# Optimization experiments

Measured on AMD Instinct MI355X. Metric: run time of the kernel, lower is better.

## Reference

```python
import jax, jax.numpy as jnp
import numpy as np

BETA = 0.25
EPS = 1e-10


def setup_inputs() -> dict:
    key = jax.random.key(0)
    k1, k2 = jax.random.split(key)
    z = jax.random.normal(k1, (16, 256, 32, 32), dtype=jnp.float32)
    # Original init: uniform(-1/n_embed, 1/n_embed)
    n_embed, embed_dim = 8192, 256
    codebook = jax.random.uniform(k2, (n_embed, embed_dim), dtype=jnp.float32,
                                  minval=-1.0 / n_embed, maxval=1.0 / n_embed)
    return {"z": z, "codebook": codebook}


def reference(z, codebook):
    B, C, H, W = z.shape
    n_embed = codebook.shape[0]
    zp = jnp.transpose(z, (0, 2, 3, 1))            # (B,H,W,C)
    zf = zp.reshape(-1, C)                          # (N,C)
    # squared L2 distances (N, n_embed)
    d = (jnp.sum(zf * zf, axis=1, keepdims=True)
         + jnp.sum(codebook * codebook, axis=1)
         - 2.0 * zf @ codebook.T)
    idx = jnp.argmin(d, axis=1)                     # (N,)
    zq = codebook[idx].reshape(zp.shape)            # gather == one-hot @ codebook
    commitment_loss = jnp.mean((jax.lax.stop_gradient(zq) - zp) ** 2)
    embedding_loss = jnp.mean((zq - jax.lax.stop_gradient(zp)) ** 2)
    loss = embedding_loss + BETA * commitment_loss
    # straight-through estimator
    zq_st = zp + jax.lax.stop_gradient(zq - zp)
    # perplexity from mean one-hot usage (counts / N)
    counts = jnp.zeros((n_embed,), dtype=zf.dtype).at[idx].add(1.0)
    avg_probs = counts / zf.shape[0]
    perplexity = jnp.exp(-jnp.sum(avg_probs * jnp.log(avg_probs + EPS)))
    zq_out = jnp.transpose(zq_st, (0, 3, 1, 2))     # (B,C,H,W)
    return zq_out, loss, perplexity, idx
```

## Files before the change

kernel.cpp:

```cpp
#include <hip/hip_runtime.h>
#include <math.h>

#define Nrows 16384
#define NE 8192
#define Kdim 256
#define HWsz 1024
#define NSPL 4
#define BETAF 0.25f
#define NLOSSBLK 4096

typedef __attribute__((ext_vector_type(8))) short bf16x8;
typedef __attribute__((ext_vector_type(16))) float f32x16;
typedef unsigned short u16;

__device__ inline u16 bf16_rne(float x) {
  unsigned int u = __float_as_uint(x);
  return (u16)((u + 0x7FFFu + ((u >> 16) & 1u)) >> 16);
}
__device__ inline float bf16_tof(u16 h) {
  return __uint_as_float(((unsigned int)h) << 16);
}
__device__ inline void gll16(const void* g, void* l) {
  __builtin_amdgcn_global_load_lds(
      (const __attribute__((address_space(1))) unsigned int*)g,
      (__attribute__((address_space(3))) unsigned int*)l, 16, 0, 0);
}

__global__ __launch_bounds__(256) void cc_kernel(const float* __restrict__ cb,
                                                 float* __restrict__ cc) {
  int wave = threadIdx.x >> 6;
  int lane = threadIdx.x & 63;
  int row = blockIdx.x * 4 + wave;
  const float4 v = *(const float4*)(cb + (size_t)row * Kdim + lane * 4);
  float s = v.x * v.x + v.y * v.y + v.z * v.z + v.w * v.w;
  for (int off = 32; off; off >>= 1) s += __shfl_down(s, off);
  if (lane == 0) cc[row] = s;
}

__global__ __launch_bounds__(256) void conv_cb(const float* __restrict__ cb,
                                               u16* __restrict__ Cf) {
  const int g = blockIdx.x * 256 + threadIdx.x;
  const int j = g >> 4, k16 = g & 15;
  const float* src = cb + (size_t)j * Kdim + k16 * 16;
  float f[16];
#pragma unroll
  for (int q = 0; q < 4; ++q) {
    const float4 v = ((const float4*)src)[q];
    f[q * 4 + 0] = v.x; f[q * 4 + 1] = v.y; f[q * 4 + 2] = v.z; f[q * 4 + 3] = v.w;
  }
  u16 h[3][16];
#pragma unroll
  for (int i = 0; i < 16; ++i) {
    const u16 q0 = bf16_rne(f[i]);
    const float r1 = f[i] - bf16_tof(q0);
    const u16 q1 = bf16_rne(r1);
    const float r2 = r1 - bf16_tof(q1);
    h[0][i] = q0; h[1][i] = q1; h[2][i] = bf16_rne(r2);
  }
  const int j32 = j >> 5, li = j & 31;
#pragma unroll
  for (int arr = 0; arr < 3; ++arr) {
#pragma unroll
    for (int kh = 0; kh < 2; ++kh) {
      const size_t off = ((size_t)(j32 * 3 + arr) * 16 + k16) * 512 + (kh * 32 + li) * 8;
      *(int4*)(Cf + off) = *(int4*)&h[arr][kh * 8];
    }
  }
}

__global__ __launch_bounds__(256) void conv_z(const float* __restrict__ z,
                                              u16* __restrict__ Zf,
                                              float* __restrict__ zz) {
  __shared__ float tile[64][68];
  const int t = threadIdx.x;
  const int bid = blockIdx.x;
  const int n0 = bid * 64;
  const int b = bid >> 4;
  const int hw0 = (bid & 15) << 6;
  const float* zb = z + (size_t)b * (Kdim * HWsz) + hw0;
  float zzacc = 0.f;
  const int rr = t >> 2;
  const int kq = (t & 3) * 16;
  for (int kc = 0; kc < 4; ++kc) {
#pragma unroll
    for (int i = 0; i < 16; ++i) {
      const int idx = i * 256 + t;
      const int k = idx >> 6, r = idx & 63;
      tile[r][k] = zb[(size_t)(kc * 64 + k) * HWsz + r];
    }
    __syncthreads();
    if (t < 64) {
      for (int k = 0; k < 64; ++k) {
        const float a = tile[t][k];
        zzacc = fmaf(a, a, zzacc);
      }
    }
    u16 h[3][16];
#pragma unroll
    for (int i = 0; i < 16; ++i) {
      const float fv = tile[rr][kq + i];
      const u16 q0 = bf16_rne(fv);
      const float r1 = fv - bf16_tof(q0);
      const u16 q1 = bf16_rne(r1);
      const float r2 = r1 - bf16_tof(q1);
      h[0][i] = q0; h[1][i] = q1; h[2][i] = bf16_rne(r2);
    }
    const int k16 = kc * 4 + (t & 3);
    const int n32 = bid * 2 + (rr >> 5), li = rr & 31;
#pragma unroll
    for (int arr = 0; arr < 3; ++arr) {
#pragma unroll
      for (int kh = 0; kh < 2; ++kh) {
        const size_t off = ((size_t)(n32 * 3 + arr) * 16 + k16) * 512 + (kh * 32 + li) * 8;
        *(int4*)(Zf + off) = *(int4*)&h[arr][kh * 8];
      }
    }
    __syncthreads();
  }
  if (t < 64) zz[n0 + t] = zzacc;
}

__global__ __launch_bounds__(256, 2) void vq_gemm(
    const u16* __restrict__ Cf, const u16* __restrict__ Zf,
    const float* __restrict__ cc, const float* __restrict__ zz,
    float* __restrict__ pd, int* __restrict__ pj) {
  __shared__ __align__(16) u16 Al[3][12288];
  __shared__ float ccs[2048];

  const int t = threadIdx.x;
  const int lane = t & 63;
  const int w = __builtin_amdgcn_readfirstlane(t >> 6);
  const int bid = blockIdx.x;
  const int cg = bid & 3;
  const int rt = bid >> 2;
  const int n32 = rt * 4 + w;

#pragma unroll
  for (int i = 0; i < 8; ++i) ccs[i * 256 + t] = cc[cg * 2048 + i * 256 + t];

  const float zzv = zz[n32 * 32 + (lane & 31)];

  bf16x8 B[16][3];
#pragma unroll
  for (int kc = 0; kc < 16; ++kc)
#pragma unroll
    for (int arr = 0; arr < 3; ++arr)
      B[kc][arr] = *(const bf16x8*)(
          Zf + ((size_t)(n32 * 3 + arr) * 16 + kc) * 512 + lane * 8);

#define STAGE(gg, c_, sl)                                                     \
  {                                                                           \
    const int ggc_ = (gg) < 32 ? (gg) : 0;                                    \
    _Pragma("unroll")                                                         \
    for (int i = 0; i < 6; ++i) {                                             \
      const int s = w * 6 + i;                                                \
      const int jx = s / 12, rem = s % 12;                                    \
      const int kc2 = rem / 3, arr = rem % 3;                                 \
      gll16(Cf + ((size_t)((cg * 64 + ggc_ * 2 + jx) * 3 + arr) * 16 +        \
                  ((c_) * 4 + kc2)) * 512 + lane * 8,                         \
            &Al[sl][((jx * 4 + kc2) * 3 + arr) * 512]);                       \
    }                                                                         \
  }

#define MF(af, bv, ac) ac = __builtin_amdgcn_mfma_f32_32x32x16_bf16(af, bv, ac, 0, 0, 0);
#define CHUNK(sl, c_)                                                         \
  _Pragma("unroll")                                                           \
  for (int kc2 = 0; kc2 < 4; ++kc2) {                                         \
    bf16x8 a0[3], a1[3];                                                      \
    _Pragma("unroll")                                                         \
    for (int arr = 0; arr < 3; ++arr) {                                       \
      a0[arr] = *(const bf16x8*)&Al[sl][(kc2 * 3 + arr) * 512 + lane * 8];    \
      a1[arr] = *(const bf16x8*)&Al[sl][((4 + kc2) * 3 + arr) * 512 + lane * 8]; \
    }                                                                         \
    MF(a0[0], B[(c_) * 4 + kc2][0], acc0) MF(a1[0], B[(c_) * 4 + kc2][0], acc1) \
    MF(a0[0], B[(c_) * 4 + kc2][1], acc0) MF(a1[0], B[(c_) * 4 + kc2][1], acc1) \
    MF(a0[1], B[(c_) * 4 + kc2][0], acc0) MF(a1[1], B[(c_) * 4 + kc2][0], acc1) \
    MF(a0[1], B[(c_) * 4 + kc2][1], acc0) MF(a1[1], B[(c_) * 4 + kc2][1], acc1) \
    MF(a0[0], B[(c_) * 4 + kc2][2], acc0) MF(a1[0], B[(c_) * 4 + kc2][2], acc1) \
    MF(a0[2], B[(c_) * 4 + kc2][0], acc0) MF(a1[2], B[(c_) * 4 + kc2][0], acc1) \
  }

#define WTB()                                                                 \
  __builtin_amdgcn_sched_barrier(0);                                          \
  asm volatile("s_waitcnt vmcnt(6)" ::: "memory");                            \
  __builtin_amdgcn_s_barrier();                                               \
  __builtin_amdgcn_sched_barrier(0);

#define ROT() { sl = (sl == 2) ? 0 : sl + 1; s2 = (s2 == 2) ? 0 : s2 + 1; }

  STAGE(0, 0, 0)
  STAGE(0, 1, 1)
  asm volatile("s_waitcnt lgkmcnt(0)" ::: "memory");
  __builtin_amdgcn_sched_barrier(0);

  float bd = INFINITY;
  int bj = 0;
  const f32x16 zero16 = {0,0,0,0,0,0,0,0,0,0,0,0,0,0,0,0};
  int sl = 0, s2 = 2;

  for (int g = 0; g < 32; ++g) {
    f32x16 acc0 = zero16, acc1 = zero16;
    WTB() STAGE(g, 2, s2)     CHUNK(sl, 0) ROT()
    WTB() STAGE(g, 3, s2)     CHUNK(sl, 1) ROT()
    WTB() STAGE(g + 1, 0, s2) CHUNK(sl, 2) ROT()
    WTB() STAGE(g + 1, 1, s2) CHUNK(sl, 3) ROT()

#pragma unroll
    for (int jx = 0; jx < 2; ++jx) {
      const f32x16& a = jx ? acc1 : acc0;
#pragma unroll
      for (int q = 0; q < 4; ++q) {
        const float4 c4 = *(const float4*)&ccs[g * 64 + jx * 32 + q * 8 + (lane >> 5) * 4];
        const float cv[4] = {c4.x, c4.y, c4.z, c4.w};
#pragma unroll
        for (int r = 0; r < 4; ++r) {
          const float d = (zzv + cv[r]) - 2.0f * a[q * 4 + r];
          const int j = cg * 2048 + g * 64 + jx * 32 + r + q * 8 + (lane >> 5) * 4;
          if (d < bd) { bd = d; bj = j; }
        }
      }
    }
  }
  asm volatile("s_waitcnt vmcnt(0)" ::: "memory");
#undef STAGE
#undef CHUNK
#undef MF
#undef WTB
#undef ROT

  {
    const float od = __shfl_xor(bd, 32);
    const int oj = __shfl_xor(bj, 32);
    if (od < bd || (od == bd && oj < bj)) { bd = od; bj = oj; }
  }
  if (lane < 32) {
    const int n = n32 * 32 + lane;
    pd[(size_t)cg * Nrows + n] = bd;
    pj[(size_t)cg * Nrows + n] = bj;
  }
}

__global__ __launch_bounds__(256) void vq_combine(const float* __restrict__ pd,
                                                  const int* __restrict__ pj,
                                                  int* __restrict__ idx_int,
                                                  float* __restrict__ out_idxf,
                                                  int* __restrict__ counts) {
  const int n = blockIdx.x * 256 + threadIdx.x;
  float d0 = pd[n];
  int j0 = pj[n];
  for (int s = 1; s < NSPL; ++s) {
    const float d = pd[(size_t)s * Nrows + n];
    const int j = pj[(size_t)s * Nrows + n];
    if (d < d0 || (d == d0 && j < j0)) { d0 = d; j0 = j; }
  }
  idx_int[n] = j0;
  out_idxf[n] = (float)j0;
  atomicAdd(&counts[j0], 1);
}

__global__ __launch_bounds__(256) void vq_gather_loss(
    const float* __restrict__ z, const float* __restrict__ cb,
    const int* __restrict__ idx_int, float* __restrict__ outz,
    float* __restrict__ loss_part) {
  const int g = blockIdx.x * 256 + threadIdx.x;
  const int hw4 = g & 255;
  const int c = (g >> 8) & 255;
  const int b = g >> 16;
  const int n = b * HWsz + hw4 * 4;
  const float4 zv = *(const float4*)(z + (size_t)g * 4);
  const int4 j4 = *(const int4*)(idx_int + n);
  float4 q;
  q.x = cb[(size_t)j4.x * Kdim + c];
  q.y = cb[(size_t)j4.y * Kdim + c];
  q.z = cb[(size_t)j4.z * Kdim + c];
  q.w = cb[(size_t)j4.w * Kdim + c];
  *(float4*)(outz + (size_t)g * 4) = q;
  float dx = q.x - zv.x, dy = q.y - zv.y, dz = q.z - zv.z, dw = q.w - zv.w;
  float s = dx * dx + dy * dy + dz * dz + dw * dw;
  for (int off = 32; off; off >>= 1) s += __shfl_down(s, off);
  __shared__ float ws4[4];
  if ((threadIdx.x & 63) == 0) ws4[threadIdx.x >> 6] = s;
  __syncthreads();
  if (threadIdx.x == 0)
    loss_part[blockIdx.x] = (ws4[0] + ws4[1]) + (ws4[2] + ws4[3]);
}

__global__ __launch_bounds__(256) void vq_final(const int* __restrict__ counts,
                                                const float* __restrict__ loss_part,
                                                float* __restrict__ out_sc) {
  float h = 0.f;
  for (int i = threadIdx.x; i < NE; i += 256) {
    float p = (float)counts[i] * (1.0f / 16384.0f);
    h += p * logf(p + 1e-10f);
  }
  float ls = 0.f;
  for (int i = threadIdx.x; i < NLOSSBLK; i += 256) ls += loss_part[i];
  for (int off = 32; off; off >>= 1) {
    h += __shfl_down(h, off);
    ls += __shfl_down(ls, off);
  }
  __shared__ float hs[4], lss[4];
  if ((threadIdx.x & 63) == 0) {
    hs[threadIdx.x >> 6] = h;
    lss[threadIdx.x >> 6] = ls;
  }
  __syncthreads();
  if (threadIdx.x == 0) {
    float H = (hs[0] + hs[1]) + (hs[2] + hs[3]);
    float L = (lss[0] + lss[1]) + (lss[2] + lss[3]);
    float m = L * (1.0f / 4194304.0f);
    out_sc[0] = m + BETAF * m;
    out_sc[1] = expf(-H);
  }
}

extern "C" void kernel_launch(void* const* d_in, const int* in_sizes, int n_in,
                              void* d_out, int out_size, void* d_ws, size_t ws_size,
                              hipStream_t stream) {
  const float* z = (const float*)d_in[0];
  const float* cb = (const float*)d_in[1];
  float* out = (float*)d_out;
  float* out_zq = out;
  float* out_sc = out + 4194304;
  float* out_idx = out + 4194306;

  char* wp = (char*)d_ws;
  u16* Cf = (u16*)wp;           wp += (size_t)NE * Kdim * 2 * 3;
  u16* Zf = (u16*)wp;           wp += (size_t)Nrows * Kdim * 2 * 3;
  float* cc = (float*)wp;       wp += (size_t)NE * 4;
  float* zz = (float*)wp;       wp += (size_t)Nrows * 4;
  float* pd = (float*)wp;       wp += (size_t)NSPL * Nrows * 4;
  int* pj = (int*)wp;           wp += (size_t)NSPL * Nrows * 4;
  int* idx_int = (int*)wp;      wp += (size_t)Nrows * 4;
  int* counts = (int*)wp;       wp += (size_t)NE * 4;
  float* loss_part = (float*)wp; wp += (size_t)NLOSSBLK * 4;

  hipMemsetAsync(counts, 0, (size_t)NE * 4, stream);

  cc_kernel<<<NE / 4, 256, 0, stream>>>(cb, cc);
  conv_cb<<<NE * 16 / 256, 256, 0, stream>>>(cb, Cf);
  conv_z<<<Nrows / 64, 256, 0, stream>>>(z, Zf, zz);
  vq_gemm<<<512, 256, 0, stream>>>(Cf, Zf, cc, zz, pd, pj);
  vq_combine<<<Nrows / 256, 256, 0, stream>>>(pd, pj, idx_int, out_idx, counts);
  vq_gather_loss<<<NLOSSBLK, 256, 0, stream>>>(z, cb, idx_int, out_zq, loss_part);
  vq_final<<<1, 256, 0, stream>>>(counts, loss_part, out_sc);
}
```

Baseline: 428.7 us.

## Fuse split-argmin combine into gather kernel with LDS-staged codebook rows

Removes the separate combine kernel by having each gather block reduce the per-split partial minima for its 64 rows itself. Codebook rows for those indices are loaded with contiguous float4 reads into padded LDS, then transposed so z reads and zq writes run coalesced along hw instead of doing scattered per-element codebook gathers. This saves one launch and the idx round trip. In exchange, each of the four channel-quarter blocks recomputes the same combine, and the grid shrinks to 1024 blocks.

```diff
diff --git a/kernel.cpp b/kernel.cpp
--- a/kernel.cpp
+++ b/kernel.cpp
@@ -7,7 +7,7 @@
 #define HWsz 1024
 #define NSPL 4
 #define BETAF 0.25f
-#define NLOSSBLK 4096
+#define NGATHBLK 1024
 
 typedef __attribute__((ext_vector_type(8))) short bf16x8;
 typedef __attribute__((ext_vector_type(16))) float f32x16;
@@ -240,49 +240,70 @@
   }
 }
 
-__global__ __launch_bounds__(256) void vq_combine(const float* __restrict__ pd,
-                                                  const int* __restrict__ pj,
-                                                  int* __restrict__ idx_int,
-                                                  float* __restrict__ out_idxf,
-                                                  int* __restrict__ counts) {
-  const int n = blockIdx.x * 256 + threadIdx.x;
-  float d0 = pd[n];
-  int j0 = pj[n];
-  for (int s = 1; s < NSPL; ++s) {
-    const float d = pd[(size_t)s * Nrows + n];
-    const int j = pj[(size_t)s * Nrows + n];
-    if (d < d0 || (d == d0 && j < j0)) { d0 = d; j0 = j; }
-  }
-  idx_int[n] = j0;
-  out_idxf[n] = (float)j0;
-  atomicAdd(&counts[j0], 1);
-}
-
 __global__ __launch_bounds__(256) void vq_gather_loss(
     const float* __restrict__ z, const float* __restrict__ cb,
-    const int* __restrict__ idx_int, float* __restrict__ outz,
-    float* __restrict__ loss_part) {
-  const int g = blockIdx.x * 256 + threadIdx.x;
-  const int hw4 = g & 255;
-  const int c = (g >> 8) & 255;
-  const int b = g >> 16;
-  const int n = b * HWsz + hw4 * 4;
-  const float4 zv = *(const float4*)(z + (size_t)g * 4);
-  const int4 j4 = *(const int4*)(idx_int + n);
-  float4 q;
-  q.x = cb[(size_t)j4.x * Kdim + c];
-  q.y = cb[(size_t)j4.y * Kdim + c];
-  q.z = cb[(size_t)j4.z * Kdim + c];
-  q.w = cb[(size_t)j4.w * Kdim + c];
-  *(float4*)(outz + (size_t)g * 4) = q;
-  float dx = q.x - zv.x, dy = q.y - zv.y, dz = q.z - zv.z, dw = q.w - zv.w;
-  float s = dx * dx + dy * dy + dz * dz + dw * dw;
-  for (int off = 32; off; off >>= 1) s += __shfl_down(s, off);
+    const float* __restrict__ pd, const int* __restrict__ pj,
+    float* __restrict__ outz, float* __restrict__ out_idxf,
+    int* __restrict__ counts, float* __restrict__ loss_part) {
+  __shared__ float cbl[64 * 65];
+  __shared__ int jr[64];
   __shared__ float ws4[4];
-  if ((threadIdx.x & 63) == 0) ws4[threadIdx.x >> 6] = s;
+  const int t = threadIdx.x;
+  const int bid = blockIdx.x;
+  const int nt = bid >> 2;
+  const int cq = bid & 3;
+  const int b = nt >> 4;
+  const int hw0 = (nt & 15) << 6;
+  const int n0 = b * HWsz + hw0;
+
+  if (t < 64) {
+    const int n = n0 + t;
+    float d0 = pd[n];
+    int j0 = pj[n];
+    for (int s = 1; s < NSPL; ++s) {
+      const float d = pd[(size_t)s * Nrows + n];
+      const int j = pj[(size_t)s * Nrows + n];
+      if (d < d0 || (d == d0 && j < j0)) { d0 = d; j0 = j; }
+    }
+    jr[t] = j0;
+    if (cq == 0) {
+      out_idxf[n] = (float)j0;
+      atomicAdd(&counts[j0], 1);
+    }
+  }
   __syncthreads();
-  if (threadIdx.x == 0)
-    loss_part[blockIdx.x] = (ws4[0] + ws4[1]) + (ws4[2] + ws4[3]);
+
+  {
+    const int r = t >> 2;
+    const int c0 = (t & 3) * 16;
+    const int j = jr[r];
+    const float* src = cb + (size_t)j * Kdim + cq * 64 + c0;
+#pragma unroll
+    for (int q = 0; q < 4; ++q) {
+      const float4 v = ((const float4*)src)[q];
+      float* dst = &cbl[r * 65 + c0 + q * 4];
+      dst[0] = v.x; dst[1] = v.y; dst[2] = v.z; dst[3] = v.w;
+    }
+  }
+  __syncthreads();
+
+  const int w = t >> 6, lane = t & 63;
+
+  float ls = 0.f;
+  for (int k = 0; k < 16; ++k) {
+    const int cl = w * 16 + k;
+    const int c = cq * 64 + cl;
+    const float q = cbl[lane * 65 + cl];
+    const size_t gidx = ((size_t)(b * Kdim + c)) * HWsz + hw0 + lane;
+    const float zv = z[gidx];
+    outz[gidx] = q;
+    const float dd = q - zv;
+    ls = fmaf(dd, dd, ls);
+  }
+  for (int off = 32; off; off >>= 1) ls += __shfl_down(ls, off);
+  if (lane == 0) ws4[w] = ls;
+  __syncthreads();
+  if (t == 0) loss_part[bid] = (ws4[0] + ws4[1]) + (ws4[2] + ws4[3]);
 }
 
 __global__ __launch_bounds__(256) void vq_final(const int* __restrict__ counts,
@@ -294,7 +315,7 @@
     h += p * logf(p + 1e-10f);
   }
   float ls = 0.f;
-  for (int i = threadIdx.x; i < NLOSSBLK; i += 256) ls += loss_part[i];
+  for (int i = threadIdx.x; i < NGATHBLK; i += 256) ls += loss_part[i];
   for (int off = 32; off; off >>= 1) {
     h += __shfl_down(h, off);
     ls += __shfl_down(ls, off);
@@ -331,9 +352,8 @@
   float* zz = (float*)wp;       wp += (size_t)Nrows * 4;
   float* pd = (float*)wp;       wp += (size_t)NSPL * Nrows * 4;
   int* pj = (int*)wp;           wp += (size_t)NSPL * Nrows * 4;
-  int* idx_int = (int*)wp;      wp += (size_t)Nrows * 4;
   int* counts = (int*)wp;       wp += (size_t)NE * 4;
-  float* loss_part = (float*)wp; wp += (size_t)NLOSSBLK * 4;
+  float* loss_part = (float*)wp; wp += (size_t)NGATHBLK * 4;
 
   hipMemsetAsync(counts, 0, (size_t)NE * 4, stream);
 
@@ -341,7 +361,7 @@
   conv_cb<<<NE * 16 / 256, 256, 0, stream>>>(cb, Cf);
   conv_z<<<Nrows / 64, 256, 0, stream>>>(z, Zf, zz);
   vq_gemm<<<512, 256, 0, stream>>>(Cf, Zf, cc, zz, pd, pj);
-  vq_combine<<<Nrows / 256, 256, 0, stream>>>(pd, pj, idx_int, out_idx, counts);
-  vq_gather_loss<<<NLOSSBLK, 256, 0, stream>>>(z, cb, idx_int, out_zq, loss_part);
+  vq_gather_loss<<<NGATHBLK, 256, 0, stream>>>(z, cb, pd, pj, out_zq, out_idx,
+                                               counts, loss_part);
   vq_final<<<1, 256, 0, stream>>>(counts, loss_part, out_sc);
 }
```

Result: faster. 420.2 us (-2.0%).
